# Performance work log

Measured on AMD Instinct MI355X. Metric: run time of the kernel, lower is better.

The kernel has to match this reference:

```python
import jax, jax.numpy as jnp
import numpy as np

EMBED_DIM = 1024
NUM_HEADS = 16
D_K = EMBED_DIM // NUM_HEADS
B, T = 4, 2048


def setup_inputs() -> dict:
    key = jax.random.key(0)
    k_x, k_wqkv, k_wo = jax.random.split(key, 3)
    x = jax.random.normal(k_x, (B, T, EMBED_DIM), dtype=jnp.float32)
    # kaiming_normal on torch Linear weight [out,in]: std = sqrt(2/fan_in)=sqrt(2/embed_dim)
    std = np.sqrt(2.0 / EMBED_DIM).astype(np.float32)
    # store weights already transposed to [in, out] for y = x @ W + b
    W_qkv = jax.random.normal(k_wqkv, (EMBED_DIM, 3 * EMBED_DIM), dtype=jnp.float32) * std
    b_qkv = jnp.zeros((3 * EMBED_DIM,), dtype=jnp.float32)
    W_o = jax.random.normal(k_wo, (EMBED_DIM, EMBED_DIM), dtype=jnp.float32) * std
    b_o = jnp.zeros((EMBED_DIM,), dtype=jnp.float32)
    return {"x": x, "W_qkv": W_qkv, "b_qkv": b_qkv, "W_o": W_o, "b_o": b_o}


def reference(x, W_qkv, b_qkv, W_o, b_o):
    Bsz, Tlen, D = x.shape
    qkv = x @ W_qkv + b_qkv                      # [B,T,3D]
    q, k, v = jnp.split(qkv, 3, axis=-1)
    # split heads -> [B,H,T,d_k]
    def heads(t):
        return t.reshape(Bsz, Tlen, NUM_HEADS, D_K).transpose(0, 2, 1, 3)
    q, k, v = heads(q), heads(k), heads(v)
    scores = jnp.einsum('bhqd,bhkd->bhqk', q, k) / jnp.sqrt(jnp.float32(D_K))
    causal = jnp.tril(jnp.ones((Tlen, Tlen), dtype=bool))
    scores = jnp.where(causal[None, None], scores, -jnp.inf)
    attn = jax.nn.softmax(scores, axis=-1)
    out = jnp.einsum('bhqk,bhkd->bhqd', attn, v)  # [B,H,T,d_k]
    out = out.transpose(0, 2, 1, 3).reshape(Bsz, Tlen, D)
    return out @ W_o + b_o
```

## Files before the change

kernel.cpp:

```cpp
#include <hip/hip_runtime.h>
#include <hip/hip_bf16.h>
#include <math.h>

typedef unsigned short u16;
typedef __attribute__((ext_vector_type(8))) short bf16x8;
typedef __attribute__((ext_vector_type(4))) float f32x4;
typedef __attribute__((ext_vector_type(16))) float f32x16;
typedef __attribute__((ext_vector_type(4))) unsigned int u32x4;

#define BATCH 4
#define TSEQ  2048
#define HEADS 16
#define DK    64
#define EMB   1024
#define MROWS 8192
#define NQKV  3072
#define PHT   ((size_t)MROWS * EMB)

__device__ __forceinline__ u16 f2bf(float f) {
    union { float f; unsigned int i; } v;
    v.f = f;
    unsigned int x = v.i;
    return (u16)((x + 0x7FFFu + ((x >> 16) & 1u)) >> 16);
}

__device__ __forceinline__ unsigned int pk2bf(float a, float b) {
    float2 f2; f2.x = a; f2.y = b;
    union { __hip_bfloat162 h; unsigned int u; } cv;
    cv.h = __float22bfloat162_rn(f2);
    return cv.u;
}

__device__ __forceinline__ void gl2lds16(const u16* g, u16* l) {
    __builtin_amdgcn_global_load_lds(
        (const __attribute__((address_space(1))) unsigned int*)g,
        (__attribute__((address_space(3))) unsigned int*)l, 16, 0, 0);
}

__global__ __launch_bounds__(256) void convert_x(const float* __restrict__ X,
                                                 u16* __restrict__ Xb) {
    int i = (blockIdx.x * 256 + threadIdx.x) * 4;
    float4 v = *(const float4*)&X[i];
    ushort4 o;
    o.x = f2bf(v.x); o.y = f2bf(v.y); o.z = f2bf(v.z); o.w = f2bf(v.w);
    *(ushort4*)&Xb[i] = o;
}

__global__ __launch_bounds__(256) void transpose_both(const float* __restrict__ Wqkv,
                                                      const float* __restrict__ Wo,
                                                      u16* __restrict__ Wt,
                                                      u16* __restrict__ Wot) {
    __shared__ float tile[32][33];
    const int tx = threadIdx.x & 31, ty = threadIdx.x >> 5;
    const int K = 1024;
    const float* W;
    u16* D;
    int N, bx;
    if (blockIdx.x < 96) { W = Wqkv; D = Wt; N = 3072; bx = blockIdx.x; }
    else                 { W = Wo;   D = Wot; N = 1024; bx = blockIdx.x - 96; }
    const int by = blockIdx.y;
#pragma unroll
    for (int s = 0; s < 4; s++)
        tile[ty + 8 * s][tx] = W[(size_t)(by * 32 + ty + 8 * s) * N + bx * 32 + tx];
    __syncthreads();
#pragma unroll
    for (int s = 0; s < 4; s++)
        D[(size_t)(bx * 32 + ty + 8 * s) * K + by * 32 + tx] = f2bf(tile[tx][ty + 8 * s]);
}

template <int KDIM>
__device__ __forceinline__ void gemm_core256(const u16* __restrict__ A,
                                             const u16* __restrict__ Bt,
                                             u16* pool,
                                             int m0, int n0, int wm, int wn,
                                             int tid, int lo, int quad,
                                             f32x4 (&acc)[4][4]) {
    constexpr int NT = KDIM / 64;
    static_assert(NT >= 4 && (NT % 2) == 0, "NT even, >=4");

    const u16* ga[2];
    const u16* gb[4];
#pragma unroll
    for (int c = 0; c < 2; c++) {
        int chunk = c * 512 + tid, row = chunk >> 3, p = chunk & 7;
        ga[c] = A + (size_t)(m0 + row) * KDIM + (p ^ (row & 7)) * 8;
    }
#pragma unroll
    for (int c = 0; c < 4; c++) {
        int chunk = c * 512 + tid, row = chunk >> 3, p = chunk & 7;
        gb[c] = Bt + (size_t)(n0 + row) * KDIM + (p ^ (row & 7)) * 8;
    }

    auto stage = [&](int b) {
        u16* As = pool + b * 24576;
        u16* Bs = As + 8192;
#pragma unroll
        for (int c = 0; c < 2; c++) {
            gl2lds16(ga[c], As + (size_t)(c * 512 + tid) * 8);
            ga[c] += 64;
        }
#pragma unroll
        for (int c = 0; c < 4; c++) {
            gl2lds16(gb[c], Bs + (size_t)(c * 512 + tid) * 8);
            gb[c] += 64;
        }
    };

    bf16x8 afA[2][4], bwA[2][4], afB[2][4], bwB[2][4];

    auto ldfrag = [&](int b, bf16x8 (&af)[2][4], bf16x8 (&bw)[2][4]) {
        const u16* As = pool + b * 24576;
        const u16* Bs = As + 8192;
#pragma unroll
        for (int ks = 0; ks < 2; ks++) {
#pragma unroll
            for (int i = 0; i < 4; i++) {
                int r = wm + i * 16 + lo;
                af[ks][i] = *(const bf16x8*)&As[r * 64 + ((ks * 4 + quad) ^ (r & 7)) * 8];
            }
#pragma unroll
            for (int j = 0; j < 4; j++) {
                int r = wn + j * 16 + lo;
                bw[ks][j] = *(const bf16x8*)&Bs[r * 64 + ((ks * 4 + quad) ^ (r & 7)) * 8];
            }
        }
    };

    auto domfma = [&](bf16x8 (&af)[2][4], bf16x8 (&bw)[2][4]) {
        __builtin_amdgcn_sched_barrier(0);
        __builtin_amdgcn_s_setprio(1);
#pragma unroll
        for (int ks = 0; ks < 2; ks++)
#pragma unroll
            for (int i = 0; i < 4; i++)
#pragma unroll
                for (int j = 0; j < 4; j++)
                    acc[i][j] = __builtin_amdgcn_mfma_f32_16x16x32_bf16(
                        af[ks][i], bw[ks][j], acc[i][j], 0, 0, 0);
        __builtin_amdgcn_s_setprio(0);
    };

    stage(0); stage(1); stage(2);
    asm volatile("s_waitcnt vmcnt(12)" ::: "memory");
    __builtin_amdgcn_s_barrier();
    ldfrag(0, afA, bwA);

#pragma unroll
    for (int kt = 0; kt < NT; kt++) {
        if (kt < NT - 1) {
            asm volatile("s_waitcnt lgkmcnt(0)" ::: "memory");
            if (kt < NT - 2)
                asm volatile("s_waitcnt vmcnt(6)" ::: "memory");
            else
                asm volatile("s_waitcnt vmcnt(0)" ::: "memory");
            __builtin_amdgcn_s_barrier();
            if (kt + 3 < NT) stage(kt % 3);
            if (kt & 1) ldfrag((kt + 1) % 3, afA, bwA);
            else        ldfrag((kt + 1) % 3, afB, bwB);
        }
        if (kt & 1) domfma(afB, bwB);
        else        domfma(afA, bwA);
    }
}

__global__ __launch_bounds__(512, 1) void gemm1_mfma(const u16* __restrict__ A,
                                                     const u16* __restrict__ Bt,
                                                     const float* __restrict__ bias,
                                                     u16* __restrict__ qkv) {
    __shared__ u16 pool[3 * 24576];
    const int tid = threadIdx.x;
    const int lane = tid & 63, wv = tid >> 6;
    const int lo = lane & 15, quad = lane >> 4;
    int lin = blockIdx.y * 12 + blockIdx.x;
    int xcd = lin & 7, ord = lin >> 3;
    int patch = ord >> 5, loc = ord & 31;
    const int m0 = (xcd * 8 + (loc >> 2)) * 128;
    const int n0 = (patch * 4 + (loc & 3)) * 256;
    const int wm = (wv >> 2) * 64, wn = (wv & 3) * 64;
    const float scale2 = 0.18033688011112042f;
    f32x4 acc[4][4] = {};

    gemm_core256<1024>(A, Bt, pool, m0, n0, wm, wn, tid, lo, quad, acc);

    const int whichw = (n0 + wn) >> 10;
    if (whichw == 2) {
#pragma unroll
        for (int i = 0; i < 4; i++) {
            int mb = m0 + wm + i * 16 + quad * 4;
            int b = mb >> 11, t = mb & 2047;
#pragma unroll
            for (int j = 0; j < 4; j++) {
                int n = n0 + wn + j * 16 + lo;
                int rem = n & 1023;
                int h = rem >> 6, d = rem & 63;
                float bn = bias[n];
                ushort4 o;
                o.x = f2bf(acc[i][j][0] + bn);
                o.y = f2bf(acc[i][j][1] + bn);
                o.z = f2bf(acc[i][j][2] + bn);
                o.w = f2bf(acc[i][j][3] + bn);
                *(ushort4*)&qkv[2 * PHT +
                                (((size_t)(b * HEADS + h) * DK + d) * TSEQ + t)] = o;
            }
        }
    } else {
        const float sc = (whichw == 0) ? scale2 : 1.0f;
#pragma unroll
        for (int i = 0; i < 4; i++) {
#pragma unroll
            for (int r = 0; r < 4; r++) {
                int m = m0 + wm + i * 16 + quad * 4 + r;
                int b = m >> 11, t = m & 2047;
#pragma unroll
                for (int j = 0; j < 4; j++) {
                    int n = n0 + wn + j * 16 + lo;
                    float v = (acc[i][j][r] + bias[n]) * sc;
                    int rem = n & 1023;
                    int h = rem >> 6, d = rem & 63;
                    qkv[(size_t)whichw * PHT +
                        (((size_t)(b * HEADS + h) * TSEQ + t) * DK + d)] = f2bf(v);
                }
            }
        }
    }
}

__global__ __launch_bounds__(512, 1) void gemm2_mfma(const u16* __restrict__ A,
                                                     const u16* __restrict__ Bt,
                                                     const float* __restrict__ bias,
                                                     float* __restrict__ out) {
    __shared__ u16 pool[3 * 24576];
    const int tid = threadIdx.x;
    const int lane = tid & 63, wv = tid >> 6;
    const int lo = lane & 15, quad = lane >> 4;
    int lin = blockIdx.y * 4 + blockIdx.x;
    int xcd = lin & 7, ord = lin >> 3;
    const int m0 = (xcd * 8 + (ord >> 2)) * 128;
    const int n0 = (ord & 3) * 256;
    const int wm = (wv >> 2) * 64, wn = (wv & 3) * 64;
    f32x4 acc[4][4] = {};

    gemm_core256<1024>(A, Bt, pool, m0, n0, wm, wn, tid, lo, quad, acc);

#pragma unroll
    for (int i = 0; i < 4; i++) {
#pragma unroll
        for (int r = 0; r < 4; r++) {
            int m = m0 + wm + i * 16 + quad * 4 + r;
#pragma unroll
            for (int j = 0; j < 4; j++) {
                int n = n0 + wn + j * 16 + lo;
                out[(size_t)m * EMB + n] = acc[i][j][r] + bias[n];
            }
        }
    }
}

__global__ __launch_bounds__(256, 4) void attn_mfma(const u16* __restrict__ Qg,
                                                    const u16* __restrict__ Kg,
                                                    const u16* __restrict__ Vg,
                                                    u16* __restrict__ AO) {
    __shared__ u16 pool[4 * 4096];

    const int tid = threadIdx.x;
    const int lane = tid & 63, wv = tid >> 6;
    const int c = lane & 31, hf = lane >> 5;
    const int bh = blockIdx.x;
    const int qt = 15 - blockIdx.y;
    const size_t base = (size_t)bh * TSEQ * DK;
    const int b = bh >> 4, h = bh & 15;
    const int q0 = qt * 128;
    const int ktmax = 2 * qt + 1;
    const bf16x8 onesf = {0x3F80, 0x3F80, 0x3F80, 0x3F80,
                          0x3F80, 0x3F80, 0x3F80, 0x3F80};

    auto stageKV = [&](int kt2, int bufsel) {
        u16* Kd = pool + bufsel * 4096;
        u16* Vd = pool + 2 * 4096 + bufsel * 4096;
#pragma unroll
        for (int cc = 0; cc < 2; cc++) {
            int chunk = cc * 256 + tid;
            int row = chunk >> 3, p = chunk & 7;
            int pg = p ^ (row & 7);
            gl2lds16(Kg + base + (size_t)(kt2 * 64 + row) * DK + pg * 8,
                     Kd + chunk * 8);
        }
#pragma unroll
        for (int cc = 0; cc < 2; cc++) {
            int chunk = cc * 256 + tid;
            int row = chunk >> 3, p = chunk & 7;
            int pg = p ^ (row & 7);
            gl2lds16(Vg + base + (size_t)row * TSEQ + kt2 * 64 + pg * 8,
                     Vd + chunk * 8);
        }
    };

    stageKV(0, 0);
    bf16x8 bq[4];
#pragma unroll
    for (int s = 0; s < 4; s++)
        bq[s] = *(const bf16x8*)&Qg[base + (size_t)(q0 + wv * 32 + c) * DK +
                                    s * 16 + hf * 8];
    __syncthreads();

    f32x16 O0 = {}, O1 = {}, ls = {};
    const int wrow = q0 + wv * 32;

    for (int kt = 0; kt <= ktmax; kt++) {
        const int cur = kt & 1;
        if (kt) __syncthreads();
        if (kt < ktmax) stageKV(kt + 1, cur ^ 1);
        const u16* Ksc = pool + cur * 4096;
        const u16* Vtc = pool + 2 * 4096 + cur * 4096;

#pragma unroll
        for (int j = 0; j < 2; j++) {
            const int kb = kt * 64 + j * 32;
            if (kb <= wrow + 31) {
                f32x16 st = {};
#pragma unroll
                for (int s = 0; s < 4; s++) {
                    int row = j * 32 + c;
                    bf16x8 ak = *(const bf16x8*)&Ksc[row * 64 +
                                    (((s << 1) + hf) ^ (row & 7)) * 8];
                    st = __builtin_amdgcn_mfma_f32_32x32x16_bf16(
                        ak, bq[s], st, 0, 0, 0);
                }
                const bool part = (kb + 31 > wrow);
                const int thr = wrow + c - kb;
#pragma unroll
                for (int r = 0; r < 16; r++) {
                    float e = __builtin_amdgcn_exp2f(st[r]);
                    if (part) {
                        int ko = (r & 3) + 8 * (r >> 2) + 4 * hf;
                        if (ko > thr) e = 0.f;
                    }
                    st[r] = e;
                }
#pragma unroll
                for (int ks = 0; ks < 2; ks++) {
                    const int br = ks * 8;
                    unsigned int w0 = pk2bf(st[br + 0], st[br + 1]);
                    unsigned int w1 = pk2bf(st[br + 2], st[br + 3]);
                    unsigned int w2 = pk2bf(st[br + 4], st[br + 5]);
                    unsigned int w3 = pk2bf(st[br + 6], st[br + 7]);
                    asm volatile("v_permlane32_swap_b32 %0, %1"
                                 : "+v"(w0), "+v"(w2));
                    asm volatile("v_permlane32_swap_b32 %0, %1"
                                 : "+v"(w1), "+v"(w3));
                    union { u32x4 w; bf16x8 v; } pu;
                    pu.w[0] = w0; pu.w[1] = w1; pu.w[2] = w2; pu.w[3] = w3;
                    const int p0 = j * 4 + ks * 2 + hf;
                    bf16x8 bv0 = *(const bf16x8*)&Vtc[c * 64 +
                                    (p0 ^ (c & 7)) * 8];
                    bf16x8 bv1 = *(const bf16x8*)&Vtc[(32 + c) * 64 +
                                    (p0 ^ (c & 7)) * 8];
                    O0 = __builtin_amdgcn_mfma_f32_32x32x16_bf16(
                        pu.v, bv0, O0, 0, 0, 0);
                    O1 = __builtin_amdgcn_mfma_f32_32x32x16_bf16(
                        pu.v, bv1, O1, 0, 0, 0);
                    ls = __builtin_amdgcn_mfma_f32_32x32x16_bf16(
                        pu.v, onesf, ls, 0, 0, 0);
                }
            }
        }
    }

#pragma unroll
    for (int r = 0; r < 16; r++) {
        int qrow = q0 + wv * 32 + (r & 3) + 8 * (r >> 2) + 4 * hf;
        float inv = 1.f / ls[r];
        size_t o = (((size_t)b * TSEQ + qrow) * HEADS + h) * DK;
        AO[o + c]      = f2bf(O0[r] * inv);
        AO[o + 32 + c] = f2bf(O1[r] * inv);
    }
}

extern "C" void kernel_launch(void* const* d_in, const int* in_sizes, int n_in,
                              void* d_out, int out_size, void* d_ws, size_t ws_size,
                              hipStream_t stream) {
    const float* x    = (const float*)d_in[0];
    const float* Wqkv = (const float*)d_in[1];
    const float* bqkv = (const float*)d_in[2];
    const float* Wo   = (const float*)d_in[3];
    const float* bo   = (const float*)d_in[4];
    float* out = (float*)d_out;

    u16* Xb  = (u16*)d_ws;
    u16* Wt  = Xb + PHT;
    u16* Wot = Wt + (size_t)NQKV * EMB;
    u16* qkv = Wot + (size_t)EMB * EMB;
    u16* AO  = Xb;

    convert_x<<<MROWS * EMB / 1024, 256, 0, stream>>>(x, Xb);
    transpose_both<<<dim3(96 + 32, 32), 256, 0, stream>>>(Wqkv, Wo, Wt, Wot);

    gemm1_mfma<<<dim3(NQKV / 256, MROWS / 128), 512, 0, stream>>>(Xb, Wt, bqkv, qkv);
    attn_mfma<<<dim3(BATCH * HEADS, 16), 256, 0, stream>>>(
        qkv, qkv + PHT, qkv + 2 * PHT, AO);
    gemm2_mfma<<<dim3(EMB / 256, MROWS / 128), 512, 0, stream>>>(AO, Wot, bo, out);
}
```

Before: 235.0 us.

## Double attention query tile per wave to reuse K/V loads across two row blocks

```diff
diff --git a/kernel.cpp b/kernel.cpp
--- a/kernel.cpp
+++ b/kernel.cpp
@@ -256,7 +256,7 @@
     }
 }
 
-__global__ __launch_bounds__(256, 4) void attn_mfma(const u16* __restrict__ Qg,
+__global__ __launch_bounds__(256, 2) void attn_mfma(const u16* __restrict__ Qg,
                                                     const u16* __restrict__ Kg,
                                                     const u16* __restrict__ Vg,
                                                     u16* __restrict__ AO) {
@@ -266,11 +266,11 @@
     const int lane = tid & 63, wv = tid >> 6;
     const int c = lane & 31, hf = lane >> 5;
     const int bh = blockIdx.x;
-    const int qt = 15 - blockIdx.y;
+    const int qslot = (blockIdx.y < 4) ? 7 - blockIdx.y : blockIdx.y - 4;
     const size_t base = (size_t)bh * TSEQ * DK;
     const int b = bh >> 4, h = bh & 15;
-    const int q0 = qt * 128;
-    const int ktmax = 2 * qt + 1;
+    const int q0 = qslot * 256;
+    const int ktmax = 4 * qslot + 3;
     const bf16x8 onesf = {0x3F80, 0x3F80, 0x3F80, 0x3F80,
                           0x3F80, 0x3F80, 0x3F80, 0x3F80};
 
@@ -296,15 +296,19 @@
     };
 
     stageKV(0, 0);
-    bf16x8 bq[4];
-#pragma unroll
-    for (int s = 0; s < 4; s++)
-        bq[s] = *(const bf16x8*)&Qg[base + (size_t)(q0 + wv * 32 + c) * DK +
-                                    s * 16 + hf * 8];
+    bf16x8 bqa[4], bqb[4];
+    const int r0 = q0 + wv * 64;
+#pragma unroll
+    for (int s = 0; s < 4; s++) {
+        bqa[s] = *(const bf16x8*)&Qg[base + (size_t)(r0 + c) * DK +
+                                     s * 16 + hf * 8];
+        bqb[s] = *(const bf16x8*)&Qg[base + (size_t)(r0 + 32 + c) * DK +
+                                     s * 16 + hf * 8];
+    }
     __syncthreads();
 
-    f32x16 O0 = {}, O1 = {}, ls = {};
-    const int wrow = q0 + wv * 32;
+    f32x16 O0a = {}, O1a = {}, lsa = {};
+    f32x16 O0b = {}, O1b = {}, lsb = {};
 
     for (int kt = 0; kt <= ktmax; kt++) {
         const int cur = kt & 1;
@@ -316,51 +320,80 @@
 #pragma unroll
         for (int j = 0; j < 2; j++) {
             const int kb = kt * 64 + j * 32;
-            if (kb <= wrow + 31) {
-                f32x16 st = {};
+            if (kb <= r0 + 63) {
+                const bool needA = (kb <= r0 + 31);
+                f32x16 sa = {}, sb = {};
 #pragma unroll
                 for (int s = 0; s < 4; s++) {
                     int row = j * 32 + c;
                     bf16x8 ak = *(const bf16x8*)&Ksc[row * 64 +
                                     (((s << 1) + hf) ^ (row & 7)) * 8];
-                    st = __builtin_amdgcn_mfma_f32_32x32x16_bf16(
-                        ak, bq[s], st, 0, 0, 0);
+                    if (needA)
+                        sa = __builtin_amdgcn_mfma_f32_32x32x16_bf16(
+                            ak, bqa[s], sa, 0, 0, 0);
+                    sb = __builtin_amdgcn_mfma_f32_32x32x16_bf16(
+                        ak, bqb[s], sb, 0, 0, 0);
                 }
-                const bool part = (kb + 31 > wrow);
-                const int thr = wrow + c - kb;
+                const bool partA = needA && (kb + 31 > r0);
+                const bool partB = (kb + 31 > r0 + 32);
+                const int thrA = r0 + c - kb;
+                const int thrB = r0 + 32 + c - kb;
 #pragma unroll
                 for (int r = 0; r < 16; r++) {
-                    float e = __builtin_amdgcn_exp2f(st[r]);
-                    if (part) {
-                        int ko = (r & 3) + 8 * (r >> 2) + 4 * hf;
-                        if (ko > thr) e = 0.f;
+                    int ko = (r & 3) + 8 * (r >> 2) + 4 * hf;
+                    if (needA) {
+                        float e = __builtin_amdgcn_exp2f(sa[r]);
+                        if (partA && ko > thrA) e = 0.f;
+                        sa[r] = e;
                     }
-                    st[r] = e;
+                    float e = __builtin_amdgcn_exp2f(sb[r]);
+                    if (partB && ko > thrB) e = 0.f;
+                    sb[r] = e;
                 }
 #pragma unroll
                 for (int ks = 0; ks < 2; ks++) {
                     const int br = ks * 8;
-                    unsigned int w0 = pk2bf(st[br + 0], st[br + 1]);
-                    unsigned int w1 = pk2bf(st[br + 2], st[br + 3]);
-                    unsigned int w2 = pk2bf(st[br + 4], st[br + 5]);
-                    unsigned int w3 = pk2bf(st[br + 6], st[br + 7]);
-                    asm volatile("v_permlane32_swap_b32 %0, %1"
-                                 : "+v"(w0), "+v"(w2));
-                    asm volatile("v_permlane32_swap_b32 %0, %1"
-                                 : "+v"(w1), "+v"(w3));
-                    union { u32x4 w; bf16x8 v; } pu;
-                    pu.w[0] = w0; pu.w[1] = w1; pu.w[2] = w2; pu.w[3] = w3;
                     const int p0 = j * 4 + ks * 2 + hf;
                     bf16x8 bv0 = *(const bf16x8*)&Vtc[c * 64 +
                                     (p0 ^ (c & 7)) * 8];
                     bf16x8 bv1 = *(const bf16x8*)&Vtc[(32 + c) * 64 +
                                     (p0 ^ (c & 7)) * 8];
-                    O0 = __builtin_amdgcn_mfma_f32_32x32x16_bf16(
-                        pu.v, bv0, O0, 0, 0, 0);
-                    O1 = __builtin_amdgcn_mfma_f32_32x32x16_bf16(
-                        pu.v, bv1, O1, 0, 0, 0);
-                    ls = __builtin_amdgcn_mfma_f32_32x32x16_bf16(
-                        pu.v, onesf, ls, 0, 0, 0);
+                    if (needA) {
+                        unsigned int w0 = pk2bf(sa[br + 0], sa[br + 1]);
+                        unsigned int w1 = pk2bf(sa[br + 2], sa[br + 3]);
+                        unsigned int w2 = pk2bf(sa[br + 4], sa[br + 5]);
+                        unsigned int w3 = pk2bf(sa[br + 6], sa[br + 7]);
+                        asm volatile("v_permlane32_swap_b32 %0, %1"
+                                     : "+v"(w0), "+v"(w2));
+                        asm volatile("v_permlane32_swap_b32 %0, %1"
+                                     : "+v"(w1), "+v"(w3));
+                        union { u32x4 w; bf16x8 v; } pu;
+                        pu.w[0] = w0; pu.w[1] = w1; pu.w[2] = w2; pu.w[3] = w3;
+                        O0a = __builtin_amdgcn_mfma_f32_32x32x16_bf16(
+                            pu.v, bv0, O0a, 0, 0, 0);
+                        O1a = __builtin_amdgcn_mfma_f32_32x32x16_bf16(
+                            pu.v, bv1, O1a, 0, 0, 0);
+                        lsa = __builtin_amdgcn_mfma_f32_32x32x16_bf16(
+                            pu.v, onesf, lsa, 0, 0, 0);
+                    }
+                    {
+                        unsigned int w0 = pk2bf(sb[br + 0], sb[br + 1]);
+                        unsigned int w1 = pk2bf(sb[br + 2], sb[br + 3]);
+                        unsigned int w2 = pk2bf(sb[br + 4], sb[br + 5]);
+                        unsigned int w3 = pk2bf(sb[br + 6], sb[br + 7]);
+                        asm volatile("v_permlane32_swap_b32 %0, %1"
+                                     : "+v"(w0), "+v"(w2));
+                        asm volatile("v_permlane32_swap_b32 %0, %1"
+                                     : "+v"(w1), "+v"(w3));
+                        union { u32x4 w; bf16x8 v; } pu;
+                        pu.w[0] = w0; pu.w[1] = w1; pu.w[2] = w2; pu.w[3] = w3;
+                        O0b = __builtin_amdgcn_mfma_f32_32x32x16_bf16(
+                            pu.v, bv0, O0b, 0, 0, 0);
+                        O1b = __builtin_amdgcn_mfma_f32_32x32x16_bf16(
+                            pu.v, bv1, O1b, 0, 0, 0);
+                        lsb = __builtin_amdgcn_mfma_f32_32x32x16_bf16(
+                            pu.v, onesf, lsb, 0, 0, 0);
+                    }
                 }
             }
         }
@@ -368,11 +401,21 @@
 
 #pragma unroll
     for (int r = 0; r < 16; r++) {
-        int qrow = q0 + wv * 32 + (r & 3) + 8 * (r >> 2) + 4 * hf;
-        float inv = 1.f / ls[r];
-        size_t o = (((size_t)b * TSEQ + qrow) * HEADS + h) * DK;
-        AO[o + c]      = f2bf(O0[r] * inv);
-        AO[o + 32 + c] = f2bf(O1[r] * inv);
+        int rr = (r & 3) + 8 * (r >> 2) + 4 * hf;
+        {
+            int qrow = r0 + rr;
+            float inv = 1.f / lsa[r];
+            size_t o = (((size_t)b * TSEQ + qrow) * HEADS + h) * DK;
+            AO[o + c]      = f2bf(O0a[r] * inv);
+            AO[o + 32 + c] = f2bf(O1a[r] * inv);
+        }
+        {
+            int qrow = r0 + 32 + rr;
+            float inv = 1.f / lsb[r];
+            size_t o = (((size_t)b * TSEQ + qrow) * HEADS + h) * DK;
+            AO[o + c]      = f2bf(O0b[r] * inv);
+            AO[o + 32 + c] = f2bf(O1b[r] * inv);
+        }
     }
 }
 
@@ -396,7 +439,7 @@
     transpose_both<<<dim3(96 + 32, 32), 256, 0, stream>>>(Wqkv, Wo, Wt, Wot);
 
     gemm1_mfma<<<dim3(NQKV / 256, MROWS / 128), 512, 0, stream>>>(Xb, Wt, bqkv, qkv);
-    attn_mfma<<<dim3(BATCH * HEADS, 16), 256, 0, stream>>>(
+    attn_mfma<<<dim3(BATCH * HEADS, 8), 256, 0, stream>>>(
         qkv, qkv + PHT, qkv + 2 * PHT, AO);
     gemm2_mfma<<<dim3(EMB / 256, MROWS / 128), 512, 0, stream>>>(AO, Wot, bo, out);
 }
```

After: 258.8 us. 10.1% more time.

## Halve GEMM K-tile to 32 and raise occupancy with smaller LDS pipeline

Applied to the files above, without the earlier changes.

```diff
diff --git a/kernel.cpp b/kernel.cpp
--- a/kernel.cpp
+++ b/kernel.cpp
@@ -69,105 +69,82 @@
 }
 
 template <int KDIM>
-__device__ __forceinline__ void gemm_core256(const u16* __restrict__ A,
+__device__ __forceinline__ void gemm_core_v4(const u16* __restrict__ A,
                                              const u16* __restrict__ Bt,
                                              u16* pool,
                                              int m0, int n0, int wm, int wn,
                                              int tid, int lo, int quad,
                                              f32x4 (&acc)[4][4]) {
-    constexpr int NT = KDIM / 64;
-    static_assert(NT >= 4 && (NT % 2) == 0, "NT even, >=4");
-
-    const u16* ga[2];
-    const u16* gb[4];
+    constexpr int NT = KDIM / 32;
+    static_assert(NT >= 4, "NT >= 4");
+
+    const u16* ga;
+    const u16* gb[2];
+    {
+        int t = tid, pair = t >> 3, s = t & 7, p2 = s ^ (pair & 7);
+        int row = pair * 2 + (p2 >> 2), p = p2 & 3;
+        ga = A + (size_t)(m0 + row) * KDIM + p * 8;
+    }
 #pragma unroll
     for (int c = 0; c < 2; c++) {
-        int chunk = c * 512 + tid, row = chunk >> 3, p = chunk & 7;
-        ga[c] = A + (size_t)(m0 + row) * KDIM + (p ^ (row & 7)) * 8;
-    }
-#pragma unroll
-    for (int c = 0; c < 4; c++) {
-        int chunk = c * 512 + tid, row = chunk >> 3, p = chunk & 7;
-        gb[c] = Bt + (size_t)(n0 + row) * KDIM + (p ^ (row & 7)) * 8;
+        int t = c * 512 + tid, pair = t >> 3, s = t & 7, p2 = s ^ (pair & 7);
+        int row = pair * 2 + (p2 >> 2), p = p2 & 3;
+        gb[c] = Bt + (size_t)(n0 + row) * KDIM + p * 8;
     }
 
     auto stage = [&](int b) {
-        u16* As = pool + b * 24576;
-        u16* Bs = As + 8192;
-#pragma unroll
-        for (int c = 0; c < 2; c++) {
-            gl2lds16(ga[c], As + (size_t)(c * 512 + tid) * 8);
-            ga[c] += 64;
-        }
-#pragma unroll
-        for (int c = 0; c < 4; c++) {
-            gl2lds16(gb[c], Bs + (size_t)(c * 512 + tid) * 8);
-            gb[c] += 64;
-        }
+        u16* As = pool + b * 12288;
+        u16* Bs = As + 4096;
+        gl2lds16(ga, As + (size_t)tid * 8);            ga += 32;
+        gl2lds16(gb[0], Bs + (size_t)tid * 8);         gb[0] += 32;
+        gl2lds16(gb[1], Bs + (size_t)(512 + tid) * 8); gb[1] += 32;
     };
 
-    bf16x8 afA[2][4], bwA[2][4], afB[2][4], bwB[2][4];
-
-    auto ldfrag = [&](int b, bf16x8 (&af)[2][4], bf16x8 (&bw)[2][4]) {
-        const u16* As = pool + b * 24576;
-        const u16* Bs = As + 8192;
-#pragma unroll
-        for (int ks = 0; ks < 2; ks++) {
-#pragma unroll
-            for (int i = 0; i < 4; i++) {
-                int r = wm + i * 16 + lo;
-                af[ks][i] = *(const bf16x8*)&As[r * 64 + ((ks * 4 + quad) ^ (r & 7)) * 8];
-            }
-#pragma unroll
-            for (int j = 0; j < 4; j++) {
-                int r = wn + j * 16 + lo;
-                bw[ks][j] = *(const bf16x8*)&Bs[r * 64 + ((ks * 4 + quad) ^ (r & 7)) * 8];
-            }
-        }
-    };
-
-    auto domfma = [&](bf16x8 (&af)[2][4], bf16x8 (&bw)[2][4]) {
+    int aoff[4], boff[4];
+#pragma unroll
+    for (int i = 0; i < 4; i++) {
+        int r = wm + i * 16 + lo;
+        aoff[i] = ((r >> 1) * 8 + (((r & 1) * 4 + quad) ^ ((r >> 1) & 7))) * 8;
+    }
+#pragma unroll
+    for (int j = 0; j < 4; j++) {
+        int r = wn + j * 16 + lo;
+        boff[j] = ((r >> 1) * 8 + (((r & 1) * 4 + quad) ^ ((r >> 1) & 7))) * 8;
+    }
+
+    stage(0); stage(1); stage(2);
+    for (int kt = 0; kt < NT; kt++) {
+        if (kt <= NT - 3)      asm volatile("s_waitcnt vmcnt(6)" ::: "memory");
+        else if (kt == NT - 2) asm volatile("s_waitcnt vmcnt(3)" ::: "memory");
+        else                   asm volatile("s_waitcnt vmcnt(0)" ::: "memory");
+        __builtin_amdgcn_s_barrier();
+        const u16* As = pool + (kt % 3) * 12288;
+        const u16* Bs = As + 4096;
+        bf16x8 af[4], bw[4];
+#pragma unroll
+        for (int i = 0; i < 4; i++) af[i] = *(const bf16x8*)&As[aoff[i]];
+#pragma unroll
+        for (int j = 0; j < 4; j++) bw[j] = *(const bf16x8*)&Bs[boff[j]];
+        asm volatile("s_waitcnt lgkmcnt(0)" ::: "memory");
+        __builtin_amdgcn_s_barrier();
+        if (kt + 3 < NT) stage(kt % 3);
         __builtin_amdgcn_sched_barrier(0);
         __builtin_amdgcn_s_setprio(1);
 #pragma unroll
-        for (int ks = 0; ks < 2; ks++)
-#pragma unroll
-            for (int i = 0; i < 4; i++)
-#pragma unroll
-                for (int j = 0; j < 4; j++)
-                    acc[i][j] = __builtin_amdgcn_mfma_f32_16x16x32_bf16(
-                        af[ks][i], bw[ks][j], acc[i][j], 0, 0, 0);
+        for (int i = 0; i < 4; i++)
+#pragma unroll
+            for (int j = 0; j < 4; j++)
+                acc[i][j] = __builtin_amdgcn_mfma_f32_16x16x32_bf16(
+                    af[i], bw[j], acc[i][j], 0, 0, 0);
         __builtin_amdgcn_s_setprio(0);
-    };
-
-    stage(0); stage(1); stage(2);
-    asm volatile("s_waitcnt vmcnt(12)" ::: "memory");
-    __builtin_amdgcn_s_barrier();
-    ldfrag(0, afA, bwA);
-
-#pragma unroll
-    for (int kt = 0; kt < NT; kt++) {
-        if (kt < NT - 1) {
-            asm volatile("s_waitcnt lgkmcnt(0)" ::: "memory");
-            if (kt < NT - 2)
-                asm volatile("s_waitcnt vmcnt(6)" ::: "memory");
-            else
-                asm volatile("s_waitcnt vmcnt(0)" ::: "memory");
-            __builtin_amdgcn_s_barrier();
-            if (kt + 3 < NT) stage(kt % 3);
-            if (kt & 1) ldfrag((kt + 1) % 3, afA, bwA);
-            else        ldfrag((kt + 1) % 3, afB, bwB);
-        }
-        if (kt & 1) domfma(afB, bwB);
-        else        domfma(afA, bwA);
-    }
-}
-
-__global__ __launch_bounds__(512, 1) void gemm1_mfma(const u16* __restrict__ A,
+    }
+}
+
+__global__ __launch_bounds__(512, 4) void gemm1_mfma(const u16* __restrict__ A,
                                                      const u16* __restrict__ Bt,
                                                      const float* __restrict__ bias,
                                                      u16* __restrict__ qkv) {
-    __shared__ u16 pool[3 * 24576];
+    __shared__ u16 pool[3 * 12288];
     const int tid = threadIdx.x;
     const int lane = tid & 63, wv = tid >> 6;
     const int lo = lane & 15, quad = lane >> 4;
@@ -180,7 +157,7 @@
     const float scale2 = 0.18033688011112042f;
     f32x4 acc[4][4] = {};
 
-    gemm_core256<1024>(A, Bt, pool, m0, n0, wm, wn, tid, lo, quad, acc);
+    gemm_core_v4<1024>(A, Bt, pool, m0, n0, wm, wn, tid, lo, quad, acc);
 
     const int whichw = (n0 + wn) >> 10;
     if (whichw == 2) {
@@ -225,11 +202,11 @@
     }
 }
 
-__global__ __launch_bounds__(512, 1) void gemm2_mfma(const u16* __restrict__ A,
+__global__ __launch_bounds__(512, 4) void gemm2_mfma(const u16* __restrict__ A,
                                                      const u16* __restrict__ Bt,
                                                      const float* __restrict__ bias,
                                                      float* __restrict__ out) {
-    __shared__ u16 pool[3 * 24576];
+    __shared__ u16 pool[3 * 12288];
     const int tid = threadIdx.x;
     const int lane = tid & 63, wv = tid >> 6;
     const int lo = lane & 15, quad = lane >> 4;
@@ -240,7 +217,7 @@
     const int wm = (wv >> 2) * 64, wn = (wv & 3) * 64;
     f32x4 acc[4][4] = {};
 
-    gemm_core256<1024>(A, Bt, pool, m0, n0, wm, wn, tid, lo, quad, acc);
+    gemm_core_v4<1024>(A, Bt, pool, m0, n0, wm, wn, tid, lo, quad, acc);
 
 #pragma unroll
     for (int i = 0; i < 4; i++) {
```

Result: no change. 234.0 us (-0.5%).

## Use 256x256 tiles with an 8-phase interleaved pipeline in QKV GEMM

Applied to the files above, without the earlier changes.

```diff
diff --git a/kernel.cpp b/kernel.cpp
--- a/kernel.cpp
+++ b/kernel.cpp
@@ -163,29 +163,118 @@
     }
 }
 
-__global__ __launch_bounds__(512, 1) void gemm1_mfma(const u16* __restrict__ A,
+template <int KDIM>
+__device__ __forceinline__ void gemm_core_8ph(const u16* __restrict__ A,
+                                              const u16* __restrict__ Bt,
+                                              u16* pool,
+                                              int m0, int n0, int wm, int wn,
+                                              int tid, int lo, int quad,
+                                              f32x4 (&acc)[8][4]) {
+    constexpr int NT = KDIM / 64;
+
+    const u16* gA[2][2];
+    const u16* gB[2][2];
+    int dstoff[2];
+#pragma unroll
+    for (int c = 0; c < 2; c++) {
+        int chunk = c * 512 + tid;
+        int row = chunk >> 3, p = chunk & 7;
+        int pg = p ^ (row & 7);
+        dstoff[c] = chunk * 8;
+#pragma unroll
+        for (int h = 0; h < 2; h++) {
+            gA[h][c] = A  + (size_t)(m0 + h * 128 + row) * KDIM + pg * 8;
+            gB[h][c] = Bt + (size_t)(n0 + h * 128 + row) * KDIM + pg * 8;
+        }
+    }
+
+    auto stageHalf = [&](int op, int kt, int h) {
+        u16* base = pool + (kt & 1) * 32768 + op * 16384 + h * 8192;
+        const u16* g0 = (op ? gB : gA)[h][0] + kt * 64;
+        const u16* g1 = (op ? gB : gA)[h][1] + kt * 64;
+        gl2lds16(g0, base + dstoff[0]);
+        gl2lds16(g1, base + dstoff[1]);
+    };
+
+    stageHalf(0, 0, 0); stageHalf(0, 0, 1);
+    stageHalf(1, 0, 0); stageHalf(1, 0, 1);
+    stageHalf(1, 1, 0); stageHalf(1, 1, 1);
+
+    bf16x8 bw[2][4];
+
+    for (int kt = 0; kt < NT; kt++) {
+        const u16* At = pool + (kt & 1) * 32768;
+        const u16* Bb = At + 16384;
+#pragma unroll
+        for (int q = 0; q < 4; q++) {
+            if (q == 0) {
+                if (kt < NT - 1) asm volatile("s_waitcnt vmcnt(4)" ::: "memory");
+                else             asm volatile("s_waitcnt vmcnt(0)" ::: "memory");
+            }
+            __builtin_amdgcn_s_barrier();
+            if (q == 0) {
+#pragma unroll
+                for (int ks = 0; ks < 2; ks++)
+#pragma unroll
+                    for (int j = 0; j < 4; j++) {
+                        int r = wn + j * 16 + lo;
+                        bw[ks][j] = *(const bf16x8*)&Bb[r * 64 +
+                                        ((ks * 4 + quad) ^ (r & 7)) * 8];
+                    }
+            }
+            bf16x8 af[2][2];
+#pragma unroll
+            for (int ks = 0; ks < 2; ks++)
+#pragma unroll
+                for (int ii = 0; ii < 2; ii++) {
+                    int r = wm + (q * 2 + ii) * 16 + lo;
+                    af[ks][ii] = *(const bf16x8*)&At[r * 64 +
+                                      ((ks * 4 + quad) ^ (r & 7)) * 8];
+                }
+            if      (q == 0 && kt + 1 < NT) stageHalf(0, kt + 1, 0);
+            else if (q == 1 && kt + 1 < NT) stageHalf(0, kt + 1, 1);
+            else if (q == 2 && kt + 2 < NT) stageHalf(1, kt + 2, 0);
+            else if (q == 3 && kt + 2 < NT) stageHalf(1, kt + 2, 1);
+            asm volatile("s_waitcnt lgkmcnt(0)" ::: "memory");
+            __builtin_amdgcn_s_barrier();
+            __builtin_amdgcn_sched_barrier(0);
+            __builtin_amdgcn_s_setprio(1);
+#pragma unroll
+            for (int ks = 0; ks < 2; ks++)
+#pragma unroll
+                for (int ii = 0; ii < 2; ii++)
+#pragma unroll
+                    for (int j = 0; j < 4; j++)
+                        acc[q * 2 + ii][j] = __builtin_amdgcn_mfma_f32_16x16x32_bf16(
+                            af[ks][ii], bw[ks][j], acc[q * 2 + ii][j], 0, 0, 0);
+            __builtin_amdgcn_s_setprio(0);
+        }
+    }
+}
+
+__global__ __launch_bounds__(512, 2) void gemm1_mfma(const u16* __restrict__ A,
                                                      const u16* __restrict__ Bt,
                                                      const float* __restrict__ bias,
                                                      u16* __restrict__ qkv) {
-    __shared__ u16 pool[3 * 24576];
+    __shared__ u16 pool[2 * 32768];
     const int tid = threadIdx.x;
     const int lane = tid & 63, wv = tid >> 6;
     const int lo = lane & 15, quad = lane >> 4;
     int lin = blockIdx.y * 12 + blockIdx.x;
     int xcd = lin & 7, ord = lin >> 3;
-    int patch = ord >> 5, loc = ord & 31;
-    const int m0 = (xcd * 8 + (loc >> 2)) * 128;
+    int patch = ord >> 4, loc = ord & 15;
+    const int m0 = (xcd * 4 + (loc >> 2)) * 256;
     const int n0 = (patch * 4 + (loc & 3)) * 256;
-    const int wm = (wv >> 2) * 64, wn = (wv & 3) * 64;
+    const int wm = (wv >> 2) * 128, wn = (wv & 3) * 64;
     const float scale2 = 0.18033688011112042f;
-    f32x4 acc[4][4] = {};
-
-    gemm_core256<1024>(A, Bt, pool, m0, n0, wm, wn, tid, lo, quad, acc);
+    f32x4 acc[8][4] = {};
+
+    gemm_core_8ph<1024>(A, Bt, pool, m0, n0, wm, wn, tid, lo, quad, acc);
 
     const int whichw = (n0 + wn) >> 10;
     if (whichw == 2) {
 #pragma unroll
-        for (int i = 0; i < 4; i++) {
+        for (int i = 0; i < 8; i++) {
             int mb = m0 + wm + i * 16 + quad * 4;
             int b = mb >> 11, t = mb & 2047;
 #pragma unroll
@@ -206,7 +295,7 @@
     } else {
         const float sc = (whichw == 0) ? scale2 : 1.0f;
 #pragma unroll
-        for (int i = 0; i < 4; i++) {
+        for (int i = 0; i < 8; i++) {
 #pragma unroll
             for (int r = 0; r < 4; r++) {
                 int m = m0 + wm + i * 16 + quad * 4 + r;
@@ -395,7 +484,7 @@
     convert_x<<<MROWS * EMB / 1024, 256, 0, stream>>>(x, Xb);
     transpose_both<<<dim3(96 + 32, 32), 256, 0, stream>>>(Wqkv, Wo, Wt, Wot);
 
-    gemm1_mfma<<<dim3(NQKV / 256, MROWS / 128), 512, 0, stream>>>(Xb, Wt, bqkv, qkv);
+    gemm1_mfma<<<dim3(NQKV / 256, MROWS / 256), 512, 0, stream>>>(Xb, Wt, bqkv, qkv);
     attn_mfma<<<dim3(BATCH * HEADS, 16), 256, 0, stream>>>(
         qkv, qkv + PHT, qkv + 2 * PHT, AO);
     gemm2_mfma<<<dim3(EMB / 256, MROWS / 128), 512, 0, stream>>>(AO, Wot, bo, out);
```

After: 241.9 us. 2.9% more time.
